# Performance work log

Measured on AMD Instinct MI355X. Metric: run time of the kernel, lower is better.

Reference implementation:

```python
import jax, jax.numpy as jnp
import numpy as np

B, S, D, H, F = 2, 4096, 768, 12, 3072
DK = D // H
EPS = 1e-6


def _ln(x, g, b):
    mu = jnp.mean(x, axis=-1, keepdims=True)
    var = jnp.mean(jnp.square(x - mu), axis=-1, keepdims=True)
    return (x - mu) * jax.lax.rsqrt(var + EPS) * g + b


def setup_inputs() -> dict:
    key = jax.random.key(0)
    ks = jax.random.split(key, 12)
    sc = 0.02
    inp = {
        "inputs_q": jax.random.normal(ks[0], (B, S, D), jnp.float32),
        "inputs_k": jax.random.normal(ks[1], (B, S, D), jnp.float32),
        "inputs_v": jax.random.normal(ks[2], (B, S, D), jnp.float32),
        "mask": jnp.ones((B, 1, 1, S), jnp.int32),
        "wq": jax.random.normal(ks[3], (D, D), jnp.float32) * sc,
        "bq": jnp.zeros((D,), jnp.float32),
        "wk": jax.random.normal(ks[4], (D, D), jnp.float32) * sc,
        "bk": jnp.zeros((D,), jnp.float32),
        "wv": jax.random.normal(ks[5], (D, D), jnp.float32) * sc,
        "bv": jnp.zeros((D,), jnp.float32),
        "wo": jax.random.normal(ks[6], (D, D), jnp.float32) * sc,
        "bo": jnp.zeros((D,), jnp.float32),
        "w1": jax.random.normal(ks[7], (D, F), jnp.float32) * sc,
        "b1": jnp.zeros((F,), jnp.float32),
        "w2": jax.random.normal(ks[8], (F, D), jnp.float32) * sc,
        "b2": jnp.zeros((D,), jnp.float32),
        "g1": jnp.ones((D,), jnp.float32),
        "be1": jnp.zeros((D,), jnp.float32),
        "g2": jnp.ones((D,), jnp.float32),
        "be2": jnp.zeros((D,), jnp.float32),
    }
    return inp


def reference(inputs_q, inputs_k, inputs_v, mask, wq, bq, wk, bk, wv, bv,
              wo, bo, w1, b1, w2, b2, g1, be1, g2, be2):
    # --- multi-head self-attention (naive, unfused as in source) ---
    q = (inputs_q @ wq + bq).reshape(B, S, H, DK).transpose(0, 2, 1, 3)  # [B,H,S,DK]
    k = (inputs_k @ wk + bk).reshape(B, S, H, DK).transpose(0, 2, 1, 3)
    v = (inputs_v @ wv + bv).reshape(B, S, H, DK).transpose(0, 2, 1, 3)
    scores = jnp.einsum("bhqd,bhkd->bhqk", q, k) / np.sqrt(DK)  # [B,H,S,S]
    scores = jnp.where(mask == 0, -jnp.inf, scores)
    attn = jax.nn.softmax(scores, axis=-1)
    ctx = jnp.einsum("bhqk,bhkd->bhqd", attn, v)
    ctx = ctx.transpose(0, 2, 1, 3).reshape(B, S, D)
    attn_out = ctx @ wo + bo
    # --- residual + LN, FFN, residual + LN (dropout p=0 -> identity) ---
    x1 = _ln(inputs_q + attn_out, g1, be1)
    ffn = jax.nn.relu(x1 @ w1 + b1) @ w2 + b2
    return _ln(x1 + ffn, g2, be2)
```

## Files before the change

kernel.cpp:

```cpp
#include <hip/hip_runtime.h>
#include <stdint.h>

#define B_ 2
#define S_ 4096
#define D_ 768
#define H_ 12
#define F_ 3072
#define DK_ 64
#define QBLK 128
#define KVB 64
#define NT (S_ / KVB)

typedef __bf16 bf16x8 __attribute__((ext_vector_type(8)));
typedef float floatx4 __attribute__((ext_vector_type(4)));
typedef float floatx16 __attribute__((ext_vector_type(16)));

__device__ __forceinline__ float bf2f(unsigned short u) {
  unsigned int x = ((unsigned int)u) << 16;
  return __builtin_bit_cast(float, x);
}
__device__ __forceinline__ unsigned short f2bf(float f) {
  unsigned int x = __builtin_bit_cast(unsigned int, f);
  x += 0x7FFFu + ((x >> 16) & 1u);
  return (unsigned short)(x >> 16);
}
__device__ __forceinline__ unsigned int cvtpk_bf16(float lo, float hi) {
  unsigned int r;
  asm("v_cvt_pk_bf16_f32 %0, %1, %2" : "=v"(r) : "v"(lo), "v"(hi));
  return r;
}

__global__ __launch_bounds__(256) void wtrans(const float* __restrict__ w,
                                              unsigned short* __restrict__ wt,
                                              int K, int N) {
  __shared__ float tile[32][33];
  const int n0 = blockIdx.x * 32, k0 = blockIdx.y * 32;
  const int tx = threadIdx.x & 31, ty8 = threadIdx.x >> 5;
#pragma unroll
  for (int r = 0; r < 4; r++)
    tile[ty8 + r * 8][tx] = w[(size_t)(k0 + ty8 + r * 8) * N + n0 + tx];
  __syncthreads();
#pragma unroll
  for (int r = 0; r < 4; r++)
    wt[(size_t)(n0 + ty8 + r * 8) * K + k0 + tx] = f2bf(tile[tx][ty8 + r * 8]);
}

__global__ __launch_bounds__(256) void cvt_bf16(const float* __restrict__ x,
                                                unsigned short* __restrict__ y, int n8) {
  const int i = blockIdx.x * 256 + threadIdx.x;
  if (i >= n8) return;
  const float4 a = ((const float4*)x)[2 * i];
  const float4 b = ((const float4*)x)[2 * i + 1];
  uint4 o;
  o.x = (unsigned int)f2bf(a.x) | ((unsigned int)f2bf(a.y) << 16);
  o.y = (unsigned int)f2bf(a.z) | ((unsigned int)f2bf(a.w) << 16);
  o.z = (unsigned int)f2bf(b.x) | ((unsigned int)f2bf(b.y) << 16);
  o.w = (unsigned int)f2bf(b.z) | ((unsigned int)f2bf(b.w) << 16);
  ((uint4*)y)[i] = o;
}

template <bool RELU, int RESID_MODE, bool OUT_BF16>
__global__ __launch_bounds__(256, 2) void gemm_lds(
    const unsigned short* __restrict__ A, const unsigned short* __restrict__ Bt,
    const float* __restrict__ bias, const void* __restrict__ residv,
    void* __restrict__ outv, int M, int N, int K) {
  __shared__ __align__(16) unsigned short As[128 * 32];
  __shared__ __align__(16) unsigned short Bs[128 * 32];
  int bx = blockIdx.x, by = blockIdx.y;
  {
    const int gx = gridDim.x;
    const int nwg = gx * gridDim.y;
    const int flat = by * gx + bx;
    const int wg = (flat & 7) * (nwg >> 3) + (flat >> 3);
    bx = wg % gx; by = wg / gx;
  }
  const int t = threadIdx.x;
  const int lane = t & 63, wave = t >> 6;
  const int m0 = by * 128, n0 = bx * 128;
  const int wm = (wave >> 1) * 64, wn = (wave & 1) * 64;
  const int rl = lane & 15, kl = (lane >> 4) * 8;
  const int srow = wave * 32 + (lane >> 2);
  const int scol = (lane & 3) * 8;

  floatx4 zf = {0.f, 0.f, 0.f, 0.f};
  floatx4 acc[4][4];
#pragma unroll
  for (int i = 0; i < 4; i++)
#pragma unroll
    for (int j = 0; j < 4; j++) acc[i][j] = zf;

  const unsigned short* Ab = A + (size_t)(m0 + srow) * K + scol;
  const unsigned short* Bb = Bt + (size_t)(n0 + srow) * K + scol;
  unsigned short* AsW = As + wave * 1024;
  unsigned short* BsW = Bs + wave * 1024;

  for (int k0 = 0; k0 < K; k0 += 32) {
    __syncthreads();
    __builtin_amdgcn_global_load_lds(Ab + k0, AsW, 16, 0, 0);
    __builtin_amdgcn_global_load_lds(Ab + (size_t)16 * K + k0, AsW + 512, 16, 0, 0);
    __builtin_amdgcn_global_load_lds(Bb + k0, BsW, 16, 0, 0);
    __builtin_amdgcn_global_load_lds(Bb + (size_t)16 * K + k0, BsW + 512, 16, 0, 0);
    __syncthreads();
    bf16x8 af[4], bff[4];
#pragma unroll
    for (int i = 0; i < 4; i++)
      af[i] = __builtin_bit_cast(bf16x8, *(const uint4*)&As[(wm + i * 16 + rl) * 32 + kl]);
#pragma unroll
    for (int j = 0; j < 4; j++)
      bff[j] = __builtin_bit_cast(bf16x8, *(const uint4*)&Bs[(wn + j * 16 + rl) * 32 + kl]);
#pragma unroll
    for (int i = 0; i < 4; i++)
#pragma unroll
      for (int j = 0; j < 4; j++)
        acc[i][j] = __builtin_amdgcn_mfma_f32_16x16x32_bf16(af[i], bff[j], acc[i][j], 0, 0, 0);
  }

  const int r0 = (lane >> 4) * 4;
#pragma unroll
  for (int i = 0; i < 4; i++) {
#pragma unroll
    for (int j = 0; j < 4; j++) {
      const int col = n0 + wn + j * 16 + rl;
      const float bv = bias[col];
#pragma unroll
      for (int r = 0; r < 4; r++) {
        const int row = m0 + wm + i * 16 + r0 + r;
        float v = acc[i][j][r] + bv;
        if (RESID_MODE == 1) v += ((const float*)residv)[(size_t)row * N + col];
        if (RESID_MODE == 2) v += bf2f(((const unsigned short*)residv)[(size_t)row * N + col]);
        if (RELU) v = v > 0.f ? v : 0.f;
        if (OUT_BF16)
          ((unsigned short*)outv)[(size_t)row * N + col] = f2bf(v);
        else
          ((float*)outv)[(size_t)row * N + col] = v;
      }
    }
  }
}

__global__ __launch_bounds__(256, 3) void flash_attn_v3(
    const unsigned short* __restrict__ qg, const unsigned short* __restrict__ kg,
    const unsigned short* __restrict__ vg, const int* __restrict__ maskg,
    unsigned short* __restrict__ ctx) {
  __shared__ __align__(16) unsigned short Ks[64][64];
  __shared__ __align__(16) unsigned short Vt[64][64];
  __shared__ float Msb[64];
  __shared__ int MsFlag;

  const int t = threadIdx.x;
  const int L = t & 63, wv = t >> 6;
  const int q5 = L & 31, h5 = L >> 5;
  const int qb = blockIdx.x, h = blockIdx.y, b = blockIdx.z;
  const size_t bS = (size_t)b * S_;
  const int hb = h * DK_;
  const unsigned short* kbase = kg + bS * D_ + hb;
  const unsigned short* vbase = vg + bS * D_ + hb;
  const int* mp = maskg + bS;

  bf16x8 bq[4];
  {
    const unsigned short* qp = qg + (bS + qb * QBLK + wv * 32 + q5) * D_ + hb + h5 * 8;
#pragma unroll
    for (int ks = 0; ks < 4; ks++)
      bq[ks] = __builtin_bit_cast(bf16x8, *(const uint4*)(qp + ks * 16));
  }

  floatx16 o0, o1;
#pragma unroll
  for (int r = 0; r < 16; r++) { o0[r] = 0.f; o1[r] = 0.f; }
  float m_ = -1e30f, l_ = 0.f;

  const int skv = t >> 2, kc = (t & 3) * 2;
  uint4 kr0, kr1, vr0, vr1;
  {
    const unsigned short* kp = kbase + (size_t)skv * D_ + kc * 8;
    const unsigned short* vp = vbase + (size_t)skv * D_ + kc * 8;
    kr0 = *(const uint4*)kp; kr1 = *(const uint4*)(kp + 8);
    vr0 = *(const uint4*)vp; vr1 = *(const uint4*)(vp + 8);
  }

  const int cshift = q5 & 7;
  const int vsh0 = (q5 & 7) ^ (q5 >> 3);
  const int vsh1 = vsh0 ^ 4;

  for (int kt = 0; kt < NT; kt++) {
    const int kv0 = kt * KVB;
    __syncthreads();
    *(uint4*)&Ks[skv][((kc) ^ (skv & 7)) * 8] = kr0;
    *(uint4*)&Ks[skv][((kc + 1) ^ (skv & 7)) * 8] = kr1;
    {
      union { uint4 u; unsigned short e[8]; } a0, a1;
      a0.u = vr0; a1.u = vr1;
#pragma unroll
      for (int e = 0; e < 8; e++) {
        const int cp0 = (((skv >> 3) ^ e ^ kc) << 3) | (skv & 7);
        const int cp1 = (((skv >> 3) ^ e ^ (kc + 1)) << 3) | (skv & 7);
        Vt[kc * 8 + e][cp0] = a0.e[e];
        Vt[kc * 8 + 8 + e][cp1] = a1.e[e];
      }
    }
    if (t < 64) {
      const int mv = mp[kv0 + t];
      Msb[t] = mv ? 0.f : -1e30f;
      const unsigned long long bal = __ballot(mv != 0);
      if (t == 0) MsFlag = (bal == ~0ull) ? 1 : 0;
    }
    __syncthreads();
    if (kt + 1 < NT) {
      const unsigned short* kp = kbase + (size_t)(kv0 + KVB + skv) * D_ + kc * 8;
      const unsigned short* vp = vbase + (size_t)(kv0 + KVB + skv) * D_ + kc * 8;
      kr0 = *(const uint4*)kp; kr1 = *(const uint4*)(kp + 8);
      vr0 = *(const uint4*)vp; vr1 = *(const uint4*)(vp + 8);
    }

    floatx16 s0, s1;
#pragma unroll
    for (int r = 0; r < 16; r++) { s0[r] = 0.f; s1[r] = 0.f; }
    __builtin_amdgcn_s_setprio(1);
#pragma unroll
    for (int ks = 0; ks < 4; ks++) {
      bf16x8 ak0 = __builtin_bit_cast(bf16x8, *(const uint4*)&Ks[q5][(((ks << 1) | h5) ^ cshift) * 8]);
      bf16x8 ak1 = __builtin_bit_cast(bf16x8, *(const uint4*)&Ks[32 + q5][(((ks << 1) | h5) ^ cshift) * 8]);
      s0 = __builtin_amdgcn_mfma_f32_32x32x16_bf16(ak0, bq[ks], s0, 0, 0, 0);
      s1 = __builtin_amdgcn_mfma_f32_32x32x16_bf16(ak1, bq[ks], s1, 0, 0, 0);
    }
    __builtin_amdgcn_s_setprio(0);

    const float csc = 0.180336880111120419f;
    if (MsFlag == 0) {
#pragma unroll
      for (int r = 0; r < 16; r++) {
        const int kvl = (r & 3) + 8 * (r >> 2) + 4 * h5;
        s0[r] = s0[r] * csc + Msb[kvl];
        s1[r] = s1[r] * csc + Msb[32 + kvl];
      }
    } else {
#pragma unroll
      for (int r = 0; r < 16; r++) { s0[r] *= csc; s1[r] *= csc; }
    }

    float v8[8];
#pragma unroll
    for (int i = 0; i < 8; i++)
      v8[i] = fmaxf(fmaxf(s0[i], s0[i + 8]), fmaxf(s1[i], s1[i + 8]));
    float rmax = fmaxf(fmaxf(fmaxf(v8[0], v8[4]), fmaxf(v8[1], v8[5])),
                       fmaxf(fmaxf(v8[2], v8[6]), fmaxf(v8[3], v8[7])));
    rmax = fmaxf(rmax, __shfl_xor(rmax, 32, 64));
    if (!__all(rmax <= m_ + 8.f)) {
      const float mn = fmaxf(fmaxf(m_, rmax), -1e29f);
      const float corr = exp2f(m_ - mn);
      m_ = mn;
      l_ *= corr;
#pragma unroll
      for (int r = 0; r < 16; r++) { o0[r] *= corr; o1[r] *= corr; }
    }
#pragma unroll
    for (int r = 0; r < 16; r++) {
      s0[r] = exp2f(s0[r] - m_);
      s1[r] = exp2f(s1[r] - m_);
    }
    float a8[8];
#pragma unroll
    for (int i = 0; i < 8; i++) a8[i] = (s0[i] + s0[i + 8]) + (s1[i] + s1[i + 8]);
    float lsum = ((a8[0] + a8[1]) + (a8[2] + a8[3])) + ((a8[4] + a8[5]) + (a8[6] + a8[7]));
    lsum += __shfl_xor(lsum, 32, 64);
    l_ += lsum;

    unsigned int w[16];
#pragma unroll
    for (int a = 0; a < 8; a++) {
      w[a] = cvtpk_bf16(s0[2 * a], s0[2 * a + 1]);
      w[8 + a] = cvtpk_bf16(s1[2 * a], s1[2 * a + 1]);
    }
#pragma unroll
    for (int ks = 0; ks < 4; ks++) {
      asm("v_permlane32_swap_b32 %0, %1" : "+v"(w[4 * ks]), "+v"(w[4 * ks + 2]));
      asm("v_permlane32_swap_b32 %0, %1" : "+v"(w[4 * ks + 1]), "+v"(w[4 * ks + 3]));
    }

    __builtin_amdgcn_s_setprio(1);
#pragma unroll
    for (int ks = 0; ks < 4; ks++) {
      const bf16x8 pa = __builtin_bit_cast(bf16x8,
          make_uint4(w[4 * ks], w[4 * ks + 1], w[4 * ks + 2], w[4 * ks + 3]));
      bf16x8 av0 = __builtin_bit_cast(bf16x8, *(const uint4*)&Vt[q5][(((ks << 1) | h5) ^ vsh0) * 8]);
      bf16x8 av1 = __builtin_bit_cast(bf16x8, *(const uint4*)&Vt[32 + q5][(((ks << 1) | h5) ^ vsh1) * 8]);
      o0 = __builtin_amdgcn_mfma_f32_32x32x16_bf16(av0, pa, o0, 0, 0, 0);
      o1 = __builtin_amdgcn_mfma_f32_32x32x16_bf16(av1, pa, o1, 0, 0, 0);
    }
    __builtin_amdgcn_s_setprio(0);
  }

  {
    const float inv = 1.f / l_;
    unsigned int ep[16];
#pragma unroll
    for (int a = 0; a < 8; a++) {
      ep[a] = cvtpk_bf16(o0[2 * a] * inv, o0[2 * a + 1] * inv);
      ep[8 + a] = cvtpk_bf16(o1[2 * a] * inv, o1[2 * a + 1] * inv);
    }
    unsigned short* crow = ctx + (bS + qb * QBLK + wv * 32 + q5) * D_ + hb;
#pragma unroll
    for (int dt = 0; dt < 2; dt++)
#pragma unroll
      for (int g4 = 0; g4 < 4; g4++)
        *(uint2*)(crow + dt * 32 + g4 * 8 + h5 * 4) =
            make_uint2(ep[dt * 8 + g4 * 2], ep[dt * 8 + g4 * 2 + 1]);
  }
}

template <bool OUT_BF16>
__global__ __launch_bounds__(256) void ln_kernel(const float* __restrict__ x,
                                                 const float* __restrict__ g,
                                                 const float* __restrict__ be,
                                                 void* __restrict__ outv) {
  __shared__ float red[4];
  const int t = threadIdx.x, lane = t & 63, wave = t >> 6;
  const size_t row = blockIdx.x;
  const float* xr = x + row * D_;
  float v0 = xr[t], v1 = xr[t + 256], v2 = xr[t + 512];
  float s = v0 + v1 + v2;
#pragma unroll
  for (int off = 32; off; off >>= 1) s += __shfl_xor(s, off, 64);
  if (lane == 0) red[wave] = s;
  __syncthreads();
  const float mu = (red[0] + red[1] + red[2] + red[3]) * (1.f / 768.f);
  __syncthreads();
  const float d0 = v0 - mu, d1 = v1 - mu, d2 = v2 - mu;
  float vs = d0 * d0 + d1 * d1 + d2 * d2;
#pragma unroll
  for (int off = 32; off; off >>= 1) vs += __shfl_xor(vs, off, 64);
  if (lane == 0) red[wave] = vs;
  __syncthreads();
  const float rs = rsqrtf((red[0] + red[1] + red[2] + red[3]) * (1.f / 768.f) + 1e-6f);
  const float r0v = d0 * rs * g[t] + be[t];
  const float r1v = d1 * rs * g[t + 256] + be[t + 256];
  const float r2v = d2 * rs * g[t + 512] + be[t + 512];
  if (OUT_BF16) {
    unsigned short* o = (unsigned short*)outv + row * D_;
    o[t] = f2bf(r0v); o[t + 256] = f2bf(r1v); o[t + 512] = f2bf(r2v);
  } else {
    float* o = (float*)outv + row * D_;
    o[t] = r0v; o[t + 256] = r1v; o[t + 512] = r2v;
  }
}

extern "C" void kernel_launch(void* const* d_in, const int* in_sizes, int n_in,
                              void* d_out, int out_size, void* d_ws, size_t ws_size,
                              hipStream_t stream) {
  const float* xq = (const float*)d_in[0];
  const float* xk = (const float*)d_in[1];
  const float* xv = (const float*)d_in[2];
  const int* mask = (const int*)d_in[3];
  const float* wq = (const float*)d_in[4];
  const float* bq = (const float*)d_in[5];
  const float* wk = (const float*)d_in[6];
  const float* bk = (const float*)d_in[7];
  const float* wv = (const float*)d_in[8];
  const float* bv = (const float*)d_in[9];
  const float* wo = (const float*)d_in[10];
  const float* bo = (const float*)d_in[11];
  const float* w1 = (const float*)d_in[12];
  const float* b1 = (const float*)d_in[13];
  const float* w2 = (const float*)d_in[14];
  const float* b2 = (const float*)d_in[15];
  const float* g1 = (const float*)d_in[16];
  const float* be1 = (const float*)d_in[17];
  const float* g2 = (const float*)d_in[18];
  const float* be2 = (const float*)d_in[19];
  float* out = (float*)d_out;
  char* ws = (char*)d_ws;

  unsigned short* WQT = (unsigned short*)(ws + 0);
  unsigned short* WKT = (unsigned short*)(ws + 1179648);
  unsigned short* WVT = (unsigned short*)(ws + 2359296);
  unsigned short* WOT = (unsigned short*)(ws + 3538944);
  unsigned short* W1T = (unsigned short*)(ws + 4718592);
  unsigned short* W2T = (unsigned short*)(ws + 9437184);
  unsigned short* XQB = (unsigned short*)(ws + 14155776);
  unsigned short* XKB = (unsigned short*)(ws + 26738688);
  unsigned short* XVB = (unsigned short*)(ws + 39321600);
  unsigned short* QB = (unsigned short*)(ws + 51904512);
  unsigned short* KB = (unsigned short*)(ws + 64487424);
  unsigned short* VB = (unsigned short*)(ws + 77070336);
  unsigned short* CTXB = (unsigned short*)(ws + 14155776);
  float* X1PRE = (float*)(ws + 51904512);
  unsigned short* X1B = (unsigned short*)(ws + 77070336);
  unsigned short* HB = (unsigned short*)(ws + 14155776);
  float* X2PRE = (float*)(ws + 89653248);

  wtrans<<<dim3(24, 24), 256, 0, stream>>>(wq, WQT, 768, 768);
  wtrans<<<dim3(24, 24), 256, 0, stream>>>(wk, WKT, 768, 768);
  wtrans<<<dim3(24, 24), 256, 0, stream>>>(wv, WVT, 768, 768);
  wtrans<<<dim3(24, 24), 256, 0, stream>>>(wo, WOT, 768, 768);
  wtrans<<<dim3(96, 24), 256, 0, stream>>>(w1, W1T, 768, 3072);
  wtrans<<<dim3(24, 96), 256, 0, stream>>>(w2, W2T, 3072, 768);

  cvt_bf16<<<3072, 256, 0, stream>>>(xq, XQB, 786432);
  cvt_bf16<<<3072, 256, 0, stream>>>(xk, XKB, 786432);
  cvt_bf16<<<3072, 256, 0, stream>>>(xv, XVB, 786432);

  gemm_lds<false, 0, true><<<dim3(6, 64), 256, 0, stream>>>(XQB, WQT, bq, nullptr, QB, 8192, 768, 768);
  gemm_lds<false, 0, true><<<dim3(6, 64), 256, 0, stream>>>(XKB, WKT, bk, nullptr, KB, 8192, 768, 768);
  gemm_lds<false, 0, true><<<dim3(6, 64), 256, 0, stream>>>(XVB, WVT, bv, nullptr, VB, 8192, 768, 768);

  flash_attn_v3<<<dim3(S_ / QBLK, H_, B_), 256, 0, stream>>>(QB, KB, VB, mask, CTXB);

  gemm_lds<false, 1, false><<<dim3(6, 64), 256, 0, stream>>>(CTXB, WOT, bo, xq, X1PRE, 8192, 768, 768);

  ln_kernel<true><<<8192, 256, 0, stream>>>(X1PRE, g1, be1, X1B);

  gemm_lds<true, 0, true><<<dim3(24, 64), 256, 0, stream>>>(X1B, W1T, b1, nullptr, HB, 8192, 3072, 768);

  gemm_lds<false, 2, false><<<dim3(6, 64), 256, 0, stream>>>(HB, W2T, b2, X1B, X2PRE, 8192, 768, 3072);

  ln_kernel<false><<<8192, 256, 0, stream>>>(X2PRE, g2, be2, out);
}
```

Baseline: 470.5 us.

## Double-buffer K/V LDS in flash attention and deepen GEMM K-tile to 64

New measurement: 472.2 us. No clear change (+0.4%).

```diff
diff --git a/kernel.cpp b/kernel.cpp
--- a/kernel.cpp
+++ b/kernel.cpp
@@ -64,8 +64,8 @@
     const unsigned short* __restrict__ A, const unsigned short* __restrict__ Bt,
     const float* __restrict__ bias, const void* __restrict__ residv,
     void* __restrict__ outv, int M, int N, int K) {
-  __shared__ __align__(16) unsigned short As[128 * 32];
-  __shared__ __align__(16) unsigned short Bs[128 * 32];
+  __shared__ __align__(16) unsigned short As[128 * 64];
+  __shared__ __align__(16) unsigned short Bs[128 * 64];
   int bx = blockIdx.x, by = blockIdx.y;
   {
     const int gx = gridDim.x;
@@ -79,8 +79,7 @@
   const int m0 = by * 128, n0 = bx * 128;
   const int wm = (wave >> 1) * 64, wn = (wave & 1) * 64;
   const int rl = lane & 15, kl = (lane >> 4) * 8;
-  const int srow = wave * 32 + (lane >> 2);
-  const int scol = (lane & 3) * 8;
+  const int lrow = lane >> 3, lcol = (lane & 7) * 8;
 
   floatx4 zf = {0.f, 0.f, 0.f, 0.f};
   floatx4 acc[4][4];
@@ -89,30 +88,34 @@
 #pragma unroll
     for (int j = 0; j < 4; j++) acc[i][j] = zf;
 
-  const unsigned short* Ab = A + (size_t)(m0 + srow) * K + scol;
-  const unsigned short* Bb = Bt + (size_t)(n0 + srow) * K + scol;
-  unsigned short* AsW = As + wave * 1024;
-  unsigned short* BsW = Bs + wave * 1024;
-
-  for (int k0 = 0; k0 < K; k0 += 32) {
+  const unsigned short* Ab = A + (size_t)(m0 + wave * 32 + lrow) * K + lcol;
+  const unsigned short* Bb = Bt + (size_t)(n0 + wave * 32 + lrow) * K + lcol;
+  unsigned short* AsW = As + wave * 2048;
+  unsigned short* BsW = Bs + wave * 2048;
+
+  for (int k0 = 0; k0 < K; k0 += 64) {
     __syncthreads();
-    __builtin_amdgcn_global_load_lds(Ab + k0, AsW, 16, 0, 0);
-    __builtin_amdgcn_global_load_lds(Ab + (size_t)16 * K + k0, AsW + 512, 16, 0, 0);
-    __builtin_amdgcn_global_load_lds(Bb + k0, BsW, 16, 0, 0);
-    __builtin_amdgcn_global_load_lds(Bb + (size_t)16 * K + k0, BsW + 512, 16, 0, 0);
+#pragma unroll
+    for (int ld = 0; ld < 4; ld++) {
+      __builtin_amdgcn_global_load_lds(Ab + k0 + (size_t)(ld * 8) * K, AsW + ld * 512, 16, 0, 0);
+      __builtin_amdgcn_global_load_lds(Bb + k0 + (size_t)(ld * 8) * K, BsW + ld * 512, 16, 0, 0);
+    }
     __syncthreads();
-    bf16x8 af[4], bff[4];
-#pragma unroll
-    for (int i = 0; i < 4; i++)
-      af[i] = __builtin_bit_cast(bf16x8, *(const uint4*)&As[(wm + i * 16 + rl) * 32 + kl]);
-#pragma unroll
-    for (int j = 0; j < 4; j++)
-      bff[j] = __builtin_bit_cast(bf16x8, *(const uint4*)&Bs[(wn + j * 16 + rl) * 32 + kl]);
-#pragma unroll
-    for (int i = 0; i < 4; i++)
+#pragma unroll
+    for (int ks = 0; ks < 2; ks++) {
+      bf16x8 af[4], bff[4];
+#pragma unroll
+      for (int i = 0; i < 4; i++)
+        af[i] = __builtin_bit_cast(bf16x8, *(const uint4*)&As[(wm + i * 16 + rl) * 64 + ks * 32 + kl]);
 #pragma unroll
       for (int j = 0; j < 4; j++)
-        acc[i][j] = __builtin_amdgcn_mfma_f32_16x16x32_bf16(af[i], bff[j], acc[i][j], 0, 0, 0);
+        bff[j] = __builtin_bit_cast(bf16x8, *(const uint4*)&Bs[(wn + j * 16 + rl) * 64 + ks * 32 + kl]);
+#pragma unroll
+      for (int i = 0; i < 4; i++)
+#pragma unroll
+        for (int j = 0; j < 4; j++)
+          acc[i][j] = __builtin_amdgcn_mfma_f32_16x16x32_bf16(af[i], bff[j], acc[i][j], 0, 0, 0);
+    }
   }
 
   const int r0 = (lane >> 4) * 4;
@@ -138,14 +141,13 @@
   }
 }
 
-__global__ __launch_bounds__(256, 3) void flash_attn_v3(
+__global__ __launch_bounds__(256, 3) void flash_attn_v4(
     const unsigned short* __restrict__ qg, const unsigned short* __restrict__ kg,
     const unsigned short* __restrict__ vg, const int* __restrict__ maskg,
     unsigned short* __restrict__ ctx) {
-  __shared__ __align__(16) unsigned short Ks[64][64];
-  __shared__ __align__(16) unsigned short Vt[64][64];
-  __shared__ float Msb[64];
-  __shared__ int MsFlag;
+  __shared__ __align__(16) unsigned short Ks[2][64][64];
+  __shared__ __align__(16) unsigned short Vt[2][64][64];
+  __shared__ unsigned char TFlag[NT];
 
   const int t = threadIdx.x;
   const int L = t & 63, wv = t >> 6;
@@ -157,6 +159,12 @@
   const unsigned short* vbase = vg + bS * D_ + hb;
   const int* mp = maskg + bS;
 
+  for (int tt = wv; tt < NT; tt += 4) {
+    const int mv = mp[tt * KVB + L];
+    const unsigned long long bal = __ballot(mv != 0);
+    if (L == 0) TFlag[tt] = (bal == ~0ull) ? 1 : 0;
+  }
+
   bf16x8 bq[4];
   {
     const unsigned short* qp = qg + (bS + qb * QBLK + wv * 32 + q5) * D_ + hb + h5 * 8;
@@ -171,41 +179,33 @@
   float m_ = -1e30f, l_ = 0.f;
 
   const int skv = t >> 2, kc = (t & 3) * 2;
+  const int cshift = q5 & 7;
+  const int vsh0 = (q5 & 7) ^ (q5 >> 3);
+  const int vsh1 = vsh0 ^ 4;
+
   uint4 kr0, kr1, vr0, vr1;
   {
     const unsigned short* kp = kbase + (size_t)skv * D_ + kc * 8;
     const unsigned short* vp = vbase + (size_t)skv * D_ + kc * 8;
     kr0 = *(const uint4*)kp; kr1 = *(const uint4*)(kp + 8);
     vr0 = *(const uint4*)vp; vr1 = *(const uint4*)(vp + 8);
-  }
-
-  const int cshift = q5 & 7;
-  const int vsh0 = (q5 & 7) ^ (q5 >> 3);
-  const int vsh1 = vsh0 ^ 4;
+    *(uint4*)&Ks[0][skv][((kc) ^ (skv & 7)) * 8] = kr0;
+    *(uint4*)&Ks[0][skv][((kc + 1) ^ (skv & 7)) * 8] = kr1;
+    union { uint4 u; unsigned short e[8]; } a0, a1;
+    a0.u = vr0; a1.u = vr1;
+#pragma unroll
+    for (int e = 0; e < 8; e++) {
+      const int cp0 = (((skv >> 3) ^ e ^ kc) << 3) | (skv & 7);
+      const int cp1 = (((skv >> 3) ^ e ^ (kc + 1)) << 3) | (skv & 7);
+      Vt[0][kc * 8 + e][cp0] = a0.e[e];
+      Vt[0][kc * 8 + 8 + e][cp1] = a1.e[e];
+    }
+  }
+  __syncthreads();
 
   for (int kt = 0; kt < NT; kt++) {
+    const int cur = kt & 1;
     const int kv0 = kt * KVB;
-    __syncthreads();
-    *(uint4*)&Ks[skv][((kc) ^ (skv & 7)) * 8] = kr0;
-    *(uint4*)&Ks[skv][((kc + 1) ^ (skv & 7)) * 8] = kr1;
-    {
-      union { uint4 u; unsigned short e[8]; } a0, a1;
-      a0.u = vr0; a1.u = vr1;
-#pragma unroll
-      for (int e = 0; e < 8; e++) {
-        const int cp0 = (((skv >> 3) ^ e ^ kc) << 3) | (skv & 7);
-        const int cp1 = (((skv >> 3) ^ e ^ (kc + 1)) << 3) | (skv & 7);
-        Vt[kc * 8 + e][cp0] = a0.e[e];
-        Vt[kc * 8 + 8 + e][cp1] = a1.e[e];
-      }
-    }
-    if (t < 64) {
-      const int mv = mp[kv0 + t];
-      Msb[t] = mv ? 0.f : -1e30f;
-      const unsigned long long bal = __ballot(mv != 0);
-      if (t == 0) MsFlag = (bal == ~0ull) ? 1 : 0;
-    }
-    __syncthreads();
     if (kt + 1 < NT) {
       const unsigned short* kp = kbase + (size_t)(kv0 + KVB + skv) * D_ + kc * 8;
       const unsigned short* vp = vbase + (size_t)(kv0 + KVB + skv) * D_ + kc * 8;
@@ -219,24 +219,24 @@
     __builtin_amdgcn_s_setprio(1);
 #pragma unroll
     for (int ks = 0; ks < 4; ks++) {
-      bf16x8 ak0 = __builtin_bit_cast(bf16x8, *(const uint4*)&Ks[q5][(((ks << 1) | h5) ^ cshift) * 8]);
-      bf16x8 ak1 = __builtin_bit_cast(bf16x8, *(const uint4*)&Ks[32 + q5][(((ks << 1) | h5) ^ cshift) * 8]);
+      bf16x8 ak0 = __builtin_bit_cast(bf16x8, *(const uint4*)&Ks[cur][q5][(((ks << 1) | h5) ^ cshift) * 8]);
+      bf16x8 ak1 = __builtin_bit_cast(bf16x8, *(const uint4*)&Ks[cur][32 + q5][(((ks << 1) | h5) ^ cshift) * 8]);
       s0 = __builtin_amdgcn_mfma_f32_32x32x16_bf16(ak0, bq[ks], s0, 0, 0, 0);
       s1 = __builtin_amdgcn_mfma_f32_32x32x16_bf16(ak1, bq[ks], s1, 0, 0, 0);
     }
     __builtin_amdgcn_s_setprio(0);
 
     const float csc = 0.180336880111120419f;
-    if (MsFlag == 0) {
+    if (TFlag[kt]) {
+#pragma unroll
+      for (int r = 0; r < 16; r++) { s0[r] *= csc; s1[r] *= csc; }
+    } else {
 #pragma unroll
       for (int r = 0; r < 16; r++) {
         const int kvl = (r & 3) + 8 * (r >> 2) + 4 * h5;
-        s0[r] = s0[r] * csc + Msb[kvl];
-        s1[r] = s1[r] * csc + Msb[32 + kvl];
+        s0[r] = s0[r] * csc + (mp[kv0 + kvl] ? 0.f : -1e30f);
+        s1[r] = s1[r] * csc + (mp[kv0 + 32 + kvl] ? 0.f : -1e30f);
       }
-    } else {
-#pragma unroll
-      for (int r = 0; r < 16; r++) { s0[r] *= csc; s1[r] *= csc; }
     }
 
     float v8[8];
@@ -283,12 +283,27 @@
     for (int ks = 0; ks < 4; ks++) {
       const bf16x8 pa = __builtin_bit_cast(bf16x8,
           make_uint4(w[4 * ks], w[4 * ks + 1], w[4 * ks + 2], w[4 * ks + 3]));
-      bf16x8 av0 = __builtin_bit_cast(bf16x8, *(const uint4*)&Vt[q5][(((ks << 1) | h5) ^ vsh0) * 8]);
-      bf16x8 av1 = __builtin_bit_cast(bf16x8, *(const uint4*)&Vt[32 + q5][(((ks << 1) | h5) ^ vsh1) * 8]);
+      bf16x8 av0 = __builtin_bit_cast(bf16x8, *(const uint4*)&Vt[cur][q5][(((ks << 1) | h5) ^ vsh0) * 8]);
+      bf16x8 av1 = __builtin_bit_cast(bf16x8, *(const uint4*)&Vt[cur][32 + q5][(((ks << 1) | h5) ^ vsh1) * 8]);
       o0 = __builtin_amdgcn_mfma_f32_32x32x16_bf16(av0, pa, o0, 0, 0, 0);
       o1 = __builtin_amdgcn_mfma_f32_32x32x16_bf16(av1, pa, o1, 0, 0, 0);
     }
     __builtin_amdgcn_s_setprio(0);
+
+    if (kt + 1 < NT) {
+      *(uint4*)&Ks[cur ^ 1][skv][((kc) ^ (skv & 7)) * 8] = kr0;
+      *(uint4*)&Ks[cur ^ 1][skv][((kc + 1) ^ (skv & 7)) * 8] = kr1;
+      union { uint4 u; unsigned short e[8]; } a0, a1;
+      a0.u = vr0; a1.u = vr1;
+#pragma unroll
+      for (int e = 0; e < 8; e++) {
+        const int cp0 = (((skv >> 3) ^ e ^ kc) << 3) | (skv & 7);
+        const int cp1 = (((skv >> 3) ^ e ^ (kc + 1)) << 3) | (skv & 7);
+        Vt[cur ^ 1][kc * 8 + e][cp0] = a0.e[e];
+        Vt[cur ^ 1][kc * 8 + 8 + e][cp1] = a1.e[e];
+      }
+    }
+    __syncthreads();
   }
 
   {
@@ -404,7 +419,7 @@
   gemm_lds<false, 0, true><<<dim3(6, 64), 256, 0, stream>>>(XKB, WKT, bk, nullptr, KB, 8192, 768, 768);
   gemm_lds<false, 0, true><<<dim3(6, 64), 256, 0, stream>>>(XVB, WVT, bv, nullptr, VB, 8192, 768, 768);
 
-  flash_attn_v3<<<dim3(S_ / QBLK, H_, B_), 256, 0, stream>>>(QB, KB, VB, mask, CTXB);
+  flash_attn_v4<<<dim3(S_ / QBLK, H_, B_), 256, 0, stream>>>(QB, KB, VB, mask, CTXB);
 
   gemm_lds<false, 1, false><<<dim3(6, 64), 256, 0, stream>>>(CTXB, WOT, bo, xq, X1PRE, 8192, 768, 768);
 
```
